# Kernel optimization log

Measured on AMD Instinct MI355X. Metric: run time of the kernel, lower is better.

The kernel has to match this reference:

```python
import jax, jax.numpy as jnp
import numpy as np

B, L, D, DF, E, R = 4, 1024, 1024, 4096, 32768, 64
EPS = 1e-6


def layer_norm(x, g, b, eps=EPS):
    mu = x.mean(-1, keepdims=True)
    var = ((x - mu) ** 2).mean(-1, keepdims=True)
    return (x - mu) * jax.lax.rsqrt(var + eps) * g + b


def setup_inputs() -> dict:
    key = jax.random.key(0)
    ks = jax.random.split(key, 16)
    s = 0.02
    return {
        "hidden_states": jax.random.normal(ks[0], (B, L, D), jnp.float32),
        "rel_table": jax.random.normal(ks[1], (R, D), jnp.float32) * s,
        "Wq": jax.random.normal(ks[2], (D, D), jnp.float32) * s,
        "bq": jnp.zeros((D,), jnp.float32),
        "Wk": jax.random.normal(ks[3], (D, D), jnp.float32) * s,
        "Wv": jax.random.normal(ks[4], (D, D), jnp.float32) * s,
        "Wo": jax.random.normal(ks[5], (D, D), jnp.float32) * s,
        "bo": jnp.zeros((D,), jnp.float32),
        "ln0_g": jnp.ones((D,), jnp.float32),
        "ln0_b": jnp.zeros((D,), jnp.float32),
        "ln1_g": jnp.ones((D,), jnp.float32),
        "ln1_b": jnp.zeros((D,), jnp.float32),
        "W1": jax.random.normal(ks[6], (D, DF), jnp.float32) * s,
        "b1": jnp.zeros((DF,), jnp.float32),
        "W2": jax.random.normal(ks[7], (DF, D), jnp.float32) * s,
        "b2": jnp.zeros((D,), jnp.float32),
        "ln2_g": jnp.ones((D,), jnp.float32),
        "ln2_b": jnp.zeros((D,), jnp.float32),
        "edge_src": jax.random.randint(ks[8], (B, E), 0, L, jnp.int32),
        "edge_dst": jax.random.randint(ks[9], (B, E), 0, L, jnp.int32),
        "edge_rel": jax.random.randint(ks[10], (B, E), 0, R, jnp.int32),
    }


def reference(hidden_states, rel_table, Wq, bq, Wk, Wv, Wo, bo,
              ln0_g, ln0_b, ln1_g, ln1_b, W1, b1, W2, b2, ln2_g, ln2_b,
              edge_src, edge_dst, edge_rel):
    scale = np.sqrt(D).astype(np.float32)  # num_heads=1 -> d_k = D
    hs_norm = layer_norm(hidden_states, ln0_g, ln0_b)

    def rgat_one(x, src, dst, rel):
        # x: [L, D]; src/dst/rel: [E]
        e = rel_table[rel]                       # [E, D] relation embeddings
        q = x @ Wq + bq
        k = x @ Wk
        v = x @ Wv
        score = jnp.sum((k[src] + e) * q[dst], axis=-1) / scale      # [E]
        score = jnp.exp(jnp.clip(score, -10.0, 10.0))
        wv = jax.ops.segment_sum((v[src] + e) * score[:, None], dst, num_segments=L)
        z = jax.ops.segment_sum(score, dst, num_segments=L)          # [L]
        o = wv / z[:, None]
        out = layer_norm(x + o @ Wo + bo, ln1_g, ln1_b)
        ffn = jnp.maximum(out @ W1 + b1, 0.0) @ W2 + b2
        return layer_norm(out + ffn, ln2_g, ln2_b)

    graph_rep = jax.vmap(rgat_one)(hs_norm, edge_src, edge_dst, edge_rel)
    out = jax.nn.elu(graph_rep)                  # dropout = identity (eval)
    return hidden_states + out
```

## Files before the change

kernel.cpp:

```cpp
#include <hip/hip_runtime.h>
#include <hip/hip_bf16.h>

#define B_SZ 4
#define L_SEQ 1024
#define D_MODEL 1024
#define DF_FF 4096
#define E_PER_B 32768
#define R_REL 64
#define M_ROWS (B_SZ * L_SEQ)

typedef __attribute__((ext_vector_type(8))) short bf16x8;
typedef __attribute__((ext_vector_type(4))) float f32x4;

__device__ inline float b2f(unsigned short u) {
    union { unsigned int i; float f; } x; x.i = ((unsigned int)u) << 16; return x.f;
}
__device__ inline unsigned short f2b(float f) {
    union { float f; unsigned int u; } x; x.f = f;
    unsigned int r = x.u + 0x7FFFu + ((x.u >> 16) & 1u);
    return (unsigned short)(r >> 16);
}

#define GLOBAL_CAST(p) ((const __attribute__((address_space(1))) void*)(p))
#define LDS_CAST(p)    ((__attribute__((address_space(3))) void*)(p))

#define BT_QKV (1024u * 3072u)
#define SEXT_M 1152
#define LDA_WV 1088
#define LDB_WVP 1152
#define BT_WVP (1024u * 1152u)

__global__ void prep_all(const float* __restrict__ Wq, const float* __restrict__ Wk,
                         const float* __restrict__ Wv, const float* __restrict__ Wo,
                         const float* __restrict__ W1, const float* __restrict__ W2,
                         const float* __restrict__ rel, const float* __restrict__ bq,
                         const float* __restrict__ hidden,
                         const float* __restrict__ ln0_g, const float* __restrict__ ln0_b,
                         unsigned short* __restrict__ Wqkv_t, unsigned short* __restrict__ Wo_t,
                         unsigned short* __restrict__ W1_t, unsigned short* __restrict__ W2_t,
                         unsigned short* __restrict__ relbPad,
                         float* __restrict__ bqkv,
                         unsigned short* __restrict__ Xn_b16,
                         float* __restrict__ zeroReg) {
    __shared__ float tile[32][33];
    __shared__ float sb1[4], sb2[4];
    const int id = blockIdx.x, tid = threadIdx.x;
    if (id < 12288) {
        const float* src; unsigned short* dst; int K, N, x, y;
        if (id < 4096) {
            const int seg = id >> 10, t = id & 1023;
            K = 1024; N = 1024; x = t & 31; y = t >> 5;
            src = (seg == 0) ? Wq : (seg == 1) ? Wk : (seg == 2) ? Wv : Wo;
            dst = (seg == 3) ? Wo_t : (Wqkv_t + (size_t)seg * 1048576);
        } else if (id < 8192) {
            const int t = id - 4096; K = 1024; N = 4096; x = t & 127; y = t >> 7;
            src = W1; dst = W1_t;
        } else {
            const int t = id - 8192; K = 4096; N = 1024; x = t & 31; y = t >> 5;
            src = W2; dst = W2_t;
        }
        const int n0 = x * 32, k0 = y * 32, tx = tid & 31, ty = tid >> 5;
#pragma unroll
        for (int r = 0; r < 32; r += 8)
            tile[ty + r][tx] = src[(size_t)(k0 + ty + r) * N + (n0 + tx)];
        __syncthreads();
#pragma unroll
        for (int r = 0; r < 32; r += 8)
            dst[(size_t)(n0 + ty + r) * K + (k0 + tx)] = f2b(tile[tx][ty + r]);
    } else if (id < 12800) {
        const int i = (id - 12288) * 256 + tid;
        relbPad[i] = (i < 65536) ? f2b(rel[i]) : (unsigned short)0;
    } else if (id < 12812) {
        const int i = (id - 12800) * 256 + tid;
        bqkv[i] = (i < 1024) ? bq[i] : 0.0f;
    } else if (id < 16908) {
        const int row = id - 12812, t = tid;
        const size_t base = (size_t)row * 1024 + t * 4;
        float4 xv = *(const float4*)(hidden + base);
        float x0 = xv.x, x1 = xv.y, x2 = xv.z, x3 = xv.w;
        float s = x0 + x1 + x2 + x3;
#pragma unroll
        for (int o = 32; o > 0; o >>= 1) s += __shfl_down(s, o);
        if ((t & 63) == 0) sb1[t >> 6] = s;
        __syncthreads();
        const float mu = (sb1[0] + sb1[1] + sb1[2] + sb1[3]) * (1.0f / 1024.0f);
        const float d0 = x0 - mu, d1 = x1 - mu, d2 = x2 - mu, d3 = x3 - mu;
        float s2 = d0 * d0 + d1 * d1 + d2 * d2 + d3 * d3;
#pragma unroll
        for (int o = 32; o > 0; o >>= 1) s2 += __shfl_down(s2, o);
        if ((t & 63) == 0) sb2[t >> 6] = s2;
        __syncthreads();
        const float var = (sb2[0] + sb2[1] + sb2[2] + sb2[3]) * (1.0f / 1024.0f);
        const float rstd = rsqrtf(var + 1e-6f);
        const float4 gv = *(const float4*)(ln0_g + t * 4);
        const float4 bv = *(const float4*)(ln0_b + t * 4);
        ushort4 ob;
        ob.x = f2b(d0 * rstd * gv.x + bv.x);
        ob.y = f2b(d1 * rstd * gv.y + bv.y);
        ob.z = f2b(d2 * rstd * gv.z + bv.z);
        ob.w = f2b(d3 * rstd * gv.w + bv.w);
        *(ushort4*)(Xn_b16 + base) = ob;
    } else {
        const size_t base = (size_t)(id - 16908) * 4096 + tid * 4;
        const float4 z4 = make_float4(0.f, 0.f, 0.f, 0.f);
#pragma unroll
        for (int j = 0; j < 4; j++)
            *(float4*)(zeroReg + base + j * 1024) = z4;
    }
}

__device__ inline void tile_swizzle(int id, int ntn, int& tm, int& tn) {
    tm = ((id & 7) + ((id >> 3) / ntn) * 8) * 128;
    tn = ((id >> 3) % ntn) * 128;
}
__device__ inline void tsw256(int id, int ntn, int& tm, int& tn) {
    tm = ((id & 7) + ((id >> 3) / ntn) * 8) * 256;
    tn = ((id >> 3) % ntn) * 256;
}

#define GEMM_BODY(GA, LDA_, GB, LDB_, KLEN)                                                 \
    f32x4 acc[4][4];                                                                        \
    _Pragma("unroll") for (int i = 0; i < 4; i++)                                           \
        _Pragma("unroll") for (int j = 0; j < 4; j++) acc[i][j] = (f32x4)0.0f;              \
    for (int k0 = 0; k0 < (KLEN); k0 += 64) {                                               \
        __syncthreads();                                                                    \
        _Pragma("unroll") for (int r = 0; r < 4; ++r) {                                     \
            __builtin_amdgcn_global_load_lds(GLOBAL_CAST((GA) + (size_t)r * 8 * (LDA_)),    \
                LDS_CAST(&lA[(wave * 32 + r * 8) * 64]), 16, 0, 0);                         \
            __builtin_amdgcn_global_load_lds(GLOBAL_CAST((GB) + (size_t)r * 8 * (LDB_)),    \
                LDS_CAST(&lB[(wave * 32 + r * 8) * 64]), 16, 0, 0);                         \
        }                                                                                   \
        (GA) += 64; (GB) += 64;                                                             \
        __builtin_amdgcn_s_waitcnt(0);                                                      \
        __syncthreads();                                                                    \
        _Pragma("unroll") for (int kk = 0; kk < 2; ++kk) {                                  \
            const int cb = kk * 4 + quad;                                                   \
            bf16x8 af[4], bf[4];                                                            \
            _Pragma("unroll") for (int i = 0; i < 4; i++) {                                 \
                const int ra = wm + i * 16 + l16;                                           \
                af[i] = *(const bf16x8*)&lA[ra * 64 + ((cb ^ (ra & 7)) * 8)];               \
                const int rb = wn + i * 16 + l16;                                           \
                bf[i] = *(const bf16x8*)&lB[rb * 64 + ((cb ^ (rb & 7)) * 8)];               \
            }                                                                               \
            _Pragma("unroll") for (int mi = 0; mi < 4; mi++)                                \
                _Pragma("unroll") for (int ni = 0; ni < 4; ni++)                            \
                    acc[mi][ni] = __builtin_amdgcn_mfma_f32_16x16x32_bf16(                  \
                        af[mi], bf[ni], acc[mi][ni], 0, 0, 0);                              \
        }                                                                                   \
    }

#define ST_Aq(bufc, QM, kt) { \
    _Pragma("unroll") for (int j_ = 0; j_ < 2; j_++) { \
        const int u_ = j_ * 8 + wv; \
        const int lr_ = ((u_ >> 3) * 128) + (QM) * 64 + ((u_ & 7) * 8); \
        __builtin_amdgcn_global_load_lds(GLOBAL_CAST(Ag + (size_t)lr_ * lda + (kt) * 64), \
            LDS_CAST(&ls[bufc][0][lr_ * 64]), 16, 0, 0); } }
#define ST_Bq(bufc, QN, kt) { \
    _Pragma("unroll") for (int j_ = 0; j_ < 2; j_++) { \
        const int u_ = j_ * 8 + wv; \
        const int lr_ = ((u_ >> 2) * 64) + (QN) * 32 + ((u_ & 3) * 8); \
        __builtin_amdgcn_global_load_lds(GLOBAL_CAST(Bg + (size_t)lr_ * ldb + (kt) * 64), \
            LDS_CAST(&ls[bufc][1][lr_ * 64]), 16, 0, 0); } }

#define RD_Af(bufc, QM) { \
    _Pragma("unroll") for (int m4_ = 0; m4_ < 4; m4_++) \
        _Pragma("unroll") for (int kk_ = 0; kk_ < 2; kk_++) \
            af[m4_][kk_] = *(const bf16x8*)&ls[bufc][0][ \
                (wm * 128 + (QM) * 64 + m4_ * 16 + l16) * 64 + (((kk_ * 4 + quad) ^ (l16 & 7)) * 8)]; }
#define RD_Bs(SLOT, bufc, QN) { \
    _Pragma("unroll") for (int n2_ = 0; n2_ < 2; n2_++) \
        _Pragma("unroll") for (int kk_ = 0; kk_ < 2; kk_++) \
            SLOT[n2_][kk_] = *(const bf16x8*)&ls[bufc][1][ \
                (wc * 64 + (QN) * 32 + n2_ * 16 + l16) * 64 + (((kk_ * 4 + quad) ^ (l16 & 7)) * 8)]; }

#define VM4 asm volatile("s_waitcnt vmcnt(4)" ::: "memory");
#define VM0 asm volatile("s_waitcnt vmcnt(0)" ::: "memory");

#define MMCL(QM, QN, BS) \
    __builtin_amdgcn_s_setprio(1); \
    _Pragma("unroll") for (int m4_ = 0; m4_ < 4; m4_++) \
        _Pragma("unroll") for (int n2_ = 0; n2_ < 2; n2_++) \
            _Pragma("unroll") for (int kk_ = 0; kk_ < 2; kk_++) \
                acc[(QM) * 4 + m4_][(QN) * 2 + n2_] = __builtin_amdgcn_mfma_f32_16x16x32_bf16( \
                    af[m4_][kk_], BS[n2_][kk_], acc[(QM) * 4 + m4_][(QN) * 2 + n2_], 0, 0, 0); \
    __builtin_amdgcn_s_setprio(0);

#define PH_R(bufc, QM, QN, BS, STMT, POST) { \
    STMT; \
    RD_Af(bufc, QM) \
    asm volatile("s_waitcnt lgkmcnt(0)" ::: "memory"); \
    __builtin_amdgcn_sched_barrier(0); \
    MMCL(QM, QN, BS) \
    POST; \
    __builtin_amdgcn_s_barrier(); }
#define PH_H(bufc, QM, QN, BS, STMT, POST) { \
    STMT; \
    __builtin_amdgcn_sched_barrier(0); \
    MMCL(QM, QN, BS) \
    POST; \
    __builtin_amdgcn_s_barrier(); }

template<bool RELU, bool SPLITK>
__global__ __launch_bounds__(512, 2)
void gemm256(const unsigned short* __restrict__ A, int lda,
             const unsigned short* __restrict__ Bt, int ldb,
             const float* __restrict__ bias,
             unsigned short* __restrict__ C, size_t pstride,
             int N, int Kc, int ntn) {
    __shared__ unsigned short ls[2][2][16384];
    int tile_m, tile_n;
    tsw256(blockIdx.x, ntn, tile_m, tile_n);
    const int t = threadIdx.x;
    const int wv = t >> 6, lane = t & 63;
    const int wm = wv >> 2;
    const int wc = wv & 3;
    const int quad = lane >> 4, l16 = lane & 15;
    const int srow8 = lane >> 3;
    const int schunk = ((lane & 7) ^ srow8) * 8;
    const int z = SPLITK ? blockIdx.z : 0;
    const int kofs = z * Kc;

    const unsigned short* Ag = A + (size_t)(tile_m + srow8) * lda + kofs + schunk;
    const unsigned short* Bg = Bt + (size_t)(tile_n + srow8) * ldb + kofs + schunk;

    f32x4 acc[8][4];
#pragma unroll
    for (int i = 0; i < 8; i++)
#pragma unroll
        for (int j = 0; j < 4; j++) acc[i][j] = (f32x4)0.0f;
    bf16x8 af[4][2], b0f[2][2], b1f[2][2];

    ST_Aq(0, 0, 0) ST_Aq(0, 1, 0) ST_Bq(0, 0, 0) ST_Bq(0, 1, 0)
    ST_Aq(1, 0, 1) ST_Bq(1, 1, 1) ST_Aq(1, 1, 1)
    asm volatile("s_waitcnt vmcnt(6)" ::: "memory");
    __builtin_amdgcn_s_barrier();
    RD_Bs(b0f, 0, 0) RD_Bs(b1f, 0, 1)

    const int NI = Kc >> 7;
    for (int it = 0; it < NI - 1; ++it) {
        const int t1 = 2 * it + 1, s0 = 2 * it + 2, s1 = 2 * it + 3;
        PH_R(0, 0, 0, b0f, ST_Bq(1, 0, t1), )
        PH_H(0, 0, 1, b1f, ST_Aq(0, 0, s0), )
        PH_R(0, 1, 1, b1f, ST_Bq(0, 1, s0), VM4 RD_Bs(b1f, 1, 1))
        PH_H(0, 1, 0, b0f, ST_Aq(0, 1, s0), RD_Bs(b0f, 1, 0))
        PH_R(1, 0, 0, b0f, ST_Bq(0, 0, s0), )
        PH_H(1, 0, 1, b1f, ST_Aq(1, 0, s1), )
        PH_R(1, 1, 1, b1f, ST_Bq(1, 1, s1), VM4 RD_Bs(b1f, 0, 1))
        PH_H(1, 1, 0, b0f, ST_Aq(1, 1, s1), RD_Bs(b0f, 0, 0))
    }
    {
        const int t1 = 2 * NI - 1;
        PH_R(0, 0, 0, b0f, ST_Bq(1, 0, t1), )
        PH_H(0, 0, 1, b1f, , )
        PH_R(0, 1, 1, b1f, , VM0 RD_Bs(b1f, 1, 1))
        PH_H(0, 1, 0, b0f, , RD_Bs(b0f, 1, 0))
        PH_R(1, 0, 0, b0f, , )
        PH_H(1, 0, 1, b1f, , )
        PH_R(1, 1, 1, b1f, , )
        PH_H(1, 1, 0, b0f, , )
    }

    unsigned short* Co = C + (SPLITK ? (size_t)z * pstride : 0);
#pragma unroll
    for (int mi = 0; mi < 8; mi++) {
#pragma unroll
        for (int ni = 0; ni < 4; ni++) {
            const int col = tile_n + wc * 64 + ni * 16 + l16;
            const float bv = (SPLITK && z != 0) ? 0.0f : bias[col];
#pragma unroll
            for (int r = 0; r < 4; r++) {
                const int row = tile_m + wm * 128 + mi * 16 + quad * 4 + r;
                float v = acc[mi][ni][r] + bv;
                if (RELU) v = fmaxf(v, 0.0f);
                Co[(size_t)row * N + col] = f2b(v);
            }
        }
    }
}

__global__ __launch_bounds__(256, 4)
void sext_w(const unsigned short* __restrict__ QKV,
            const unsigned short* __restrict__ relPad,
            const unsigned short* __restrict__ Wo_t,
            unsigned short* __restrict__ Pbase,
            unsigned short* __restrict__ Bwvp) {
    __shared__ unsigned short lA[128 * 64];
    __shared__ unsigned short lB[128 * 64];
    const int id = blockIdx.x, t = threadIdx.x;
    const int wave = t >> 6, lane = t & 63;
    const int wm = (wave >> 1) * 64, wn = (wave & 1) * 64;
    const int quad = lane >> 4, l16 = lane & 15;
    const int srow = lane >> 3;
    const int schunk = ((lane & 7) ^ srow) * 8;

    if (id >= 288) {
        const int t2 = id - 288;
        const int b = t2 / 72, rem = t2 % 72;
        const int tile_m = (rem / 9) * 128;
        const int tile_n = (rem % 9) * 128;
        const unsigned short* gA = Wo_t + (size_t)(tile_m + wave * 32 + srow) * 1024 + schunk;
        const int brow = tile_n + wave * 32 + srow;
        const unsigned short* gB;
        size_t ldb;
        if (tile_n < 1024) {
            gB = QKV + (size_t)b * BT_QKV + (size_t)brow * 3072 + 2048 + schunk;
            ldb = 3072;
        } else {
            gB = relPad + (size_t)(brow - 1024) * 1024 + schunk;
            ldb = 1024;
        }
        GEMM_BODY(gA, 1024, gB, ldb, 1024)
        unsigned short* P = Bwvp + (size_t)b * BT_WVP;
#pragma unroll
        for (int mi = 0; mi < 4; mi++) {
#pragma unroll
            for (int ni = 0; ni < 4; ni++) {
                const int col = tile_n + wn + ni * 16 + l16;
#pragma unroll
                for (int r = 0; r < 4; r++) {
                    const int row = tile_m + wm + mi * 16 + quad * 4 + r;
                    P[(size_t)row * LDB_WVP + col] = f2b(acc[mi][ni][r]);
                }
            }
        }
        return;
    }

    const int bx = id % 72, b = id / 72;
    const int tile_m = (bx >> 3) * 128;
    const int tile_n = (bx & 7) * 128;
    const int arow = tile_m + wave * 32 + srow;
    const unsigned short* gA;
    size_t lda;
    if (tile_m < 1024) {
        gA = QKV + (size_t)b * BT_QKV + (size_t)arow * 3072 + 1024 + schunk;
        lda = 3072;
    } else {
        gA = relPad + (size_t)(arow - 1024) * 1024 + schunk;
        lda = 1024;
    }
    const unsigned short* gB = QKV + (size_t)b * BT_QKV
                                   + (size_t)(tile_n + wave * 32 + srow) * 3072 + schunk;
    GEMM_BODY(gA, lda, gB, 3072, 1024)
    unsigned short* P = Pbase + (size_t)b * (SEXT_M * 1024);
#pragma unroll
    for (int mi = 0; mi < 4; mi++) {
#pragma unroll
        for (int ni = 0; ni < 4; ni++) {
            const int col = tile_n + wn + ni * 16 + l16;
#pragma unroll
            for (int r = 0; r < 4; r++) {
                const int row = tile_m + wm + mi * 16 + quad * 4 + r;
                P[(size_t)row * 1024 + col] = f2b(acc[mi][ni][r]);
            }
        }
    }
}

__global__ __launch_bounds__(256, 4)
void gemm_wv_splitk(const unsigned short* __restrict__ A,
                    const unsigned short* __restrict__ Bt,
                    const float* __restrict__ bias,
                    unsigned short* __restrict__ Pbase, size_t pstride) {
    __shared__ unsigned short lA[128 * 64];
    __shared__ unsigned short lB[128 * 64];
    int tile_m, tile_n;
    tile_swizzle(blockIdx.x, 8, tile_m, tile_n);
    const int z = blockIdx.z;
    const int kofs = z * 576;
    const int Kc = z ? 512 : 576;
    const int t = threadIdx.x;
    const int wave = t >> 6, lane = t & 63;
    const int wm = (wave >> 1) * 64, wn = (wave & 1) * 64;
    const int quad = lane >> 4, l16 = lane & 15;
    const int srow = lane >> 3;
    const int schunk = ((lane & 7) ^ srow) * 8;
    const unsigned short* gA = A + (size_t)(tile_m + wave * 32 + srow) * LDA_WV + kofs + schunk;
    const unsigned short* gB = Bt + (size_t)(tile_m >> 10) * BT_WVP
                                  + (size_t)(tile_n + wave * 32 + srow) * LDB_WVP + kofs + schunk;
    GEMM_BODY(gA, LDA_WV, gB, LDB_WVP, Kc)
    unsigned short* P = Pbase + (size_t)z * pstride;
#pragma unroll
    for (int mi = 0; mi < 4; mi++) {
#pragma unroll
        for (int ni = 0; ni < 4; ni++) {
            const int col = tile_n + wn + ni * 16 + l16;
            const float bv = (z == 0) ? bias[col] : 0.0f;
#pragma unroll
            for (int r = 0; r < 4; r++) {
                const int row = tile_m + wm + mi * 16 + quad * 4 + r;
                P[(size_t)row * 1024 + col] = f2b(acc[mi][ni][r] + bv);
            }
        }
    }
}

template<bool FINAL, int NR>
__global__ void ln_kernel(const unsigned short* __restrict__ Xb,
                          const unsigned short* __restrict__ Rbase, size_t rstride,
                          const float* __restrict__ g, const float* __restrict__ be,
                          unsigned short* __restrict__ ob16,
                          const float* __restrict__ hidden, float* __restrict__ fout) {
    __shared__ float sb1[4], sb2[4];
    const int row = blockIdx.x, t = threadIdx.x;
    const size_t base = (size_t)row * 1024 + t * 4;

    ushort4 xv = *(const ushort4*)(Xb + base);
    float x0 = b2f(xv.x), x1 = b2f(xv.y), x2 = b2f(xv.z), x3 = b2f(xv.w);
#pragma unroll
    for (int r = 0; r < NR; r++) {
        ushort4 rv = *(const ushort4*)(Rbase + r * rstride + base);
        x0 += b2f(rv.x); x1 += b2f(rv.y); x2 += b2f(rv.z); x3 += b2f(rv.w);
    }
    float s = x0 + x1 + x2 + x3;
#pragma unroll
    for (int o = 32; o > 0; o >>= 1) s += __shfl_down(s, o);
    if ((t & 63) == 0) sb1[t >> 6] = s;
    __syncthreads();
    const float mu = (sb1[0] + sb1[1] + sb1[2] + sb1[3]) * (1.0f / 1024.0f);

    const float d0 = x0 - mu, d1 = x1 - mu, d2 = x2 - mu, d3 = x3 - mu;
    float s2 = d0 * d0 + d1 * d1 + d2 * d2 + d3 * d3;
#pragma unroll
    for (int o = 32; o > 0; o >>= 1) s2 += __shfl_down(s2, o);
    if ((t & 63) == 0) sb2[t >> 6] = s2;
    __syncthreads();
    const float var = (sb2[0] + sb2[1] + sb2[2] + sb2[3]) * (1.0f / 1024.0f);
    const float rstd = rsqrtf(var + 1e-6f);

    const float4 gv = *(const float4*)(g + t * 4);
    const float4 bv = *(const float4*)(be + t * 4);
    const float y0 = d0 * rstd * gv.x + bv.x;
    const float y1 = d1 * rstd * gv.y + bv.y;
    const float y2 = d2 * rstd * gv.z + bv.z;
    const float y3 = d3 * rstd * gv.w + bv.w;

    if (!FINAL) {
        ushort4 ob; ob.x = f2b(y0); ob.y = f2b(y1); ob.z = f2b(y2); ob.w = f2b(y3);
        *(ushort4*)(ob16 + base) = ob;
    } else {
        const float4 hv = *(const float4*)(hidden + base);
        const float e0 = y0 > 0.0f ? y0 : expm1f(y0);
        const float e1 = y1 > 0.0f ? y1 : expm1f(y1);
        const float e2 = y2 > 0.0f ? y2 : expm1f(y2);
        const float e3 = y3 > 0.0f ? y3 : expm1f(y3);
        float4 o; o.x = hv.x + e0; o.y = hv.y + e1; o.z = hv.z + e2; o.w = hv.w + e3;
        *(float4*)(fout + base) = o;
    }
}

__global__ void edge_scatter(const unsigned short* __restrict__ S,
                             const int* __restrict__ src, const int* __restrict__ dst,
                             const int* __restrict__ rel,
                             float* __restrict__ A, float* __restrict__ G) {
    const int gg = blockIdx.x * 256 + threadIdx.x;
    const int b = gg >> 15;
    const int s = src[gg], d = dst[gg], r = rel[gg];
    const size_t sbase = ((size_t)b * SEXT_M + s) * 1024 + d;
    const size_t tbase = ((size_t)b * SEXT_M + 1024 + r) * 1024 + d;
    const float sval = b2f(S[sbase]);
    const float tval = b2f(S[tbase]);
    float sc = (sval + tval) * (1.0f / 32.0f);
    sc = expf(fminf(fmaxf(sc, -10.0f), 10.0f));
    atomicAdd(&A[((size_t)((b << 10) + d) << 10) + s], sc);
    atomicAdd(&G[((size_t)((b << 10) + d) << 6) + r], sc);
}

__global__ void normalize(const float* __restrict__ A, const float* __restrict__ G,
                          unsigned short* __restrict__ Awv) {
    __shared__ float sInv;
    const int row = blockIdx.x, t = threadIdx.x;
    float v = 0.0f;
    if (t < 64) {
        v = G[(size_t)row * 64 + t];
        float s = v;
#pragma unroll
        for (int o = 1; o < 64; o <<= 1) s += __shfl_xor(s, o);
        if (t == 0) sInv = 1.0f / s;
    }
    __syncthreads();
    const float inv = sInv;
    const size_t obase = (size_t)row * LDA_WV;
    const float4 a = *(const float4*)(A + (size_t)row * 1024 + t * 4);
    ushort4 o;
    o.x = f2b(a.x * inv); o.y = f2b(a.y * inv); o.z = f2b(a.z * inv); o.w = f2b(a.w * inv);
    *(ushort4*)(Awv + obase + t * 4) = o;
    if (t < 16) {
        const float4 gq = *(const float4*)(G + (size_t)row * 64 + t * 4);
        ushort4 og;
        og.x = f2b(gq.x * inv); og.y = f2b(gq.y * inv);
        og.z = f2b(gq.z * inv); og.w = f2b(gq.w * inv);
        *(ushort4*)(Awv + obase + 1024 + t * 4) = og;
    }
}

extern "C" void kernel_launch(void* const* d_in, const int* in_sizes, int n_in,
                              void* d_out, int out_size, void* d_ws, size_t ws_size,
                              hipStream_t stream) {
    const float* hidden  = (const float*)d_in[0];
    const float* rel_tbl = (const float*)d_in[1];
    const float* Wq = (const float*)d_in[2];
    const float* bq = (const float*)d_in[3];
    const float* Wk = (const float*)d_in[4];
    const float* Wv = (const float*)d_in[5];
    const float* Wo = (const float*)d_in[6];
    const float* bo = (const float*)d_in[7];
    const float* ln0_g = (const float*)d_in[8];
    const float* ln0_b = (const float*)d_in[9];
    const float* ln1_g = (const float*)d_in[10];
    const float* ln1_b = (const float*)d_in[11];
    const float* W1 = (const float*)d_in[12];
    const float* b1 = (const float*)d_in[13];
    const float* W2 = (const float*)d_in[14];
    const float* b2 = (const float*)d_in[15];
    const float* ln2_g = (const float*)d_in[16];
    const float* ln2_b = (const float*)d_in[17];
    const int* esrc = (const int*)d_in[18];
    const int* edst = (const int*)d_in[19];
    const int* erel = (const int*)d_in[20];
    float* out = (float*)d_out;

    char* ws = (char*)d_ws;
    const size_t MB = 1024 * 1024;
    unsigned short* Xn_b16  = (unsigned short*)(ws + 16 * MB);
    unsigned short* H1      = (unsigned short*)(ws + 0);
    unsigned short* Wqkv_t  = (unsigned short*)(ws + 24 * MB);
    unsigned short* Wo_t    = (unsigned short*)(ws + 30 * MB);
    unsigned short* W1_t    = (unsigned short*)(ws + 32 * MB);
    unsigned short* W2_t    = (unsigned short*)(ws + 40 * MB);
    unsigned short* relbPad = (unsigned short*)(ws + 48 * MB);
    float*          bqkv    = (float*)(ws + 48 * MB + 512 * 1024);
    unsigned short* QKV     = (unsigned short*)(ws + 49 * MB);
    unsigned short* Awv     = (unsigned short*)(ws + 49 * MB);
    unsigned short* Qw2H    = (unsigned short*)(ws + 49 * MB);
    unsigned short* PwoH    = (unsigned short*)(ws + 66 * MB);
    unsigned short* SxH     = (unsigned short*)(ws + 73 * MB);
    unsigned short* Bwvp    = (unsigned short*)(ws + 92 * MB);
    float*          Amat    = (float*)(ws + 101 * MB);
    float*          Gmat    = (float*)(ws + 117 * MB);
    unsigned short* Out_b16 = (unsigned short*)(ws + 113 * MB);

    const size_t PSTRIDE_H = 4u * 1024 * 1024;
    const dim3 blk(256);
    const dim3 blk512(512);

    prep_all<<<17996, blk, 0, stream>>>(Wq, Wk, Wv, Wo, W1, W2, rel_tbl, bq,
                                        hidden, ln0_g, ln0_b,
                                        Wqkv_t, Wo_t, W1_t, W2_t, relbPad, bqkv,
                                        Xn_b16, Amat);
    gemm256<false, false><<<dim3(192), blk512, 0, stream>>>(
        Xn_b16, 1024, Wqkv_t, 1024, bqkv, QKV, 0, 3072, 1024, 12);
    sext_w<<<576, blk, 0, stream>>>(QKV, relbPad, Wo_t, SxH, Bwvp);
    edge_scatter<<<512, blk, 0, stream>>>(SxH, esrc, edst, erel, Amat, Gmat);
    normalize<<<M_ROWS, blk, 0, stream>>>(Amat, Gmat, Awv);
    gemm_wv_splitk<<<dim3(256, 1, 2), blk, 0, stream>>>(Awv, Bwvp, bo, PwoH, PSTRIDE_H);
    ln_kernel<false, 2><<<M_ROWS, blk, 0, stream>>>(Xn_b16, PwoH, PSTRIDE_H, ln1_g, ln1_b,
                                                    Out_b16, nullptr, nullptr);
    gemm256<true, false><<<dim3(256), blk512, 0, stream>>>(
        Out_b16, 1024, W1_t, 1024, b1, H1, 0, 4096, 1024, 16);
    gemm256<false, true><<<dim3(64, 1, 4), blk512, 0, stream>>>(
        H1, 4096, W2_t, 4096, b2, Qw2H, PSTRIDE_H, 1024, 1024, 4);
    ln_kernel<true, 4><<<M_ROWS, blk, 0, stream>>>(Out_b16, Qw2H, PSTRIDE_H, ln2_g, ln2_b,
                                                   nullptr, hidden, out);
    (void)in_sizes; (void)n_in; (void)out_size; (void)ws_size;
}
```

Before: 348.6 us.

## Replace edge scatter with dst-bucketed gather and LDS accumulation

Result: slower. 358.4 us (+2.8%).

```diff
diff --git a/kernel.cpp b/kernel.cpp
--- a/kernel.cpp
+++ b/kernel.cpp
@@ -41,7 +41,7 @@
                          unsigned short* __restrict__ relbPad,
                          float* __restrict__ bqkv,
                          unsigned short* __restrict__ Xn_b16,
-                         float* __restrict__ zeroReg) {
+                         unsigned int* __restrict__ cnt) {
     __shared__ float tile[32][33];
     __shared__ float sb1[4], sb2[4];
     const int id = blockIdx.x, tid = threadIdx.x;
@@ -101,11 +101,98 @@
         ob.w = f2b(d3 * rstd * gv.w + bv.w);
         *(ushort4*)(Xn_b16 + base) = ob;
     } else {
-        const size_t base = (size_t)(id - 16908) * 4096 + tid * 4;
-        const float4 z4 = make_float4(0.f, 0.f, 0.f, 0.f);
+        uint4 z4; z4.x = z4.y = z4.z = z4.w = 0u;
 #pragma unroll
         for (int j = 0; j < 4; j++)
-            *(float4*)(zeroReg + base + j * 1024) = z4;
+            *(uint4*)(cnt + tid * 16 + j * 4) = z4;
+    }
+}
+
+__global__ void bucket_count(const int* __restrict__ dst, unsigned int* __restrict__ cnt) {
+    const int gg = blockIdx.x * 256 + threadIdx.x;
+    const int b = gg >> 15;
+    atomicAdd(&cnt[(b << 10) | dst[gg]], 1u);
+}
+
+__global__ void bucket_scan(const unsigned int* __restrict__ cnt,
+                            unsigned int* __restrict__ offs,
+                            unsigned int* __restrict__ cur) {
+    __shared__ unsigned int ps[1024];
+    const int t = threadIdx.x;
+    const unsigned int c0 = cnt[t * 4], c1 = cnt[t * 4 + 1];
+    const unsigned int c2 = cnt[t * 4 + 2], c3 = cnt[t * 4 + 3];
+    const unsigned int local = c0 + c1 + c2 + c3;
+    ps[t] = local;
+    __syncthreads();
+    for (int off = 1; off < 1024; off <<= 1) {
+        const unsigned int v = (t >= off) ? ps[t - off] : 0u;
+        __syncthreads();
+        ps[t] += v;
+        __syncthreads();
+    }
+    const unsigned int excl = ps[t] - local;
+    const unsigned int o0 = excl, o1 = o0 + c0, o2 = o1 + c1, o3 = o2 + c2;
+    offs[t * 4] = o0; offs[t * 4 + 1] = o1; offs[t * 4 + 2] = o2; offs[t * 4 + 3] = o3;
+    cur[t * 4] = o0;  cur[t * 4 + 1] = o1;  cur[t * 4 + 2] = o2;  cur[t * 4 + 3] = o3;
+}
+
+__global__ void bucket_fill(const int* __restrict__ src, const int* __restrict__ dst,
+                            const int* __restrict__ rel,
+                            unsigned int* __restrict__ cur, unsigned int* __restrict__ elist) {
+    const int gg = blockIdx.x * 256 + threadIdx.x;
+    const int b = gg >> 15;
+    const unsigned int pos = atomicAdd(&cur[(b << 10) | dst[gg]], 1u);
+    elist[pos] = (unsigned int)src[gg] | ((unsigned int)rel[gg] << 10);
+}
+
+__global__ void edge_gather(const unsigned short* __restrict__ S,
+                            const unsigned int* __restrict__ cnt,
+                            const unsigned int* __restrict__ offs,
+                            const unsigned int* __restrict__ elist,
+                            unsigned short* __restrict__ Awv) {
+    __shared__ float aRow[1024];
+    __shared__ float gRow[64];
+    __shared__ float sInvL;
+    const int bd = blockIdx.x;
+    const int b = bd >> 10, d = bd & 1023;
+    const int t = threadIdx.x;
+#pragma unroll
+    for (int j = 0; j < 4; j++) aRow[t * 4 + j] = 0.0f;
+    if (t < 64) gRow[t] = 0.0f;
+    __syncthreads();
+
+    const unsigned int n = cnt[bd];
+    const unsigned int base = offs[bd];
+    const size_t sB = (size_t)b * SEXT_M * 1024 + d;
+    for (unsigned int i = t; i < n; i += 256) {
+        const unsigned int e = elist[base + i];
+        const int s = e & 1023, r = e >> 10;
+        const float sval = b2f(S[sB + (size_t)s * 1024]);
+        const float tval = b2f(S[sB + (size_t)(1024 + r) * 1024]);
+        float sc = (sval + tval) * (1.0f / 32.0f);
+        sc = expf(fminf(fmaxf(sc, -10.0f), 10.0f));
+        atomicAdd(&aRow[s], sc);
+        atomicAdd(&gRow[r], sc);
+    }
+    __syncthreads();
+    if (t < 64) {
+        float s = gRow[t];
+#pragma unroll
+        for (int o = 1; o < 64; o <<= 1) s += __shfl_xor(s, o);
+        if (t == 0) sInvL = 1.0f / s;
+    }
+    __syncthreads();
+    const float inv = sInvL;
+    const size_t obase = (size_t)bd * LDA_WV;
+    ushort4 o;
+    o.x = f2b(aRow[t * 4] * inv);     o.y = f2b(aRow[t * 4 + 1] * inv);
+    o.z = f2b(aRow[t * 4 + 2] * inv); o.w = f2b(aRow[t * 4 + 3] * inv);
+    *(ushort4*)(Awv + obase + t * 4) = o;
+    if (t < 16) {
+        ushort4 og;
+        og.x = f2b(gRow[t * 4] * inv);     og.y = f2b(gRow[t * 4 + 1] * inv);
+        og.z = f2b(gRow[t * 4 + 2] * inv); og.w = f2b(gRow[t * 4 + 3] * inv);
+        *(ushort4*)(Awv + obase + 1024 + t * 4) = og;
     }
 }
 
@@ -449,51 +536,6 @@
     }
 }
 
-__global__ void edge_scatter(const unsigned short* __restrict__ S,
-                             const int* __restrict__ src, const int* __restrict__ dst,
-                             const int* __restrict__ rel,
-                             float* __restrict__ A, float* __restrict__ G) {
-    const int gg = blockIdx.x * 256 + threadIdx.x;
-    const int b = gg >> 15;
-    const int s = src[gg], d = dst[gg], r = rel[gg];
-    const size_t sbase = ((size_t)b * SEXT_M + s) * 1024 + d;
-    const size_t tbase = ((size_t)b * SEXT_M + 1024 + r) * 1024 + d;
-    const float sval = b2f(S[sbase]);
-    const float tval = b2f(S[tbase]);
-    float sc = (sval + tval) * (1.0f / 32.0f);
-    sc = expf(fminf(fmaxf(sc, -10.0f), 10.0f));
-    atomicAdd(&A[((size_t)((b << 10) + d) << 10) + s], sc);
-    atomicAdd(&G[((size_t)((b << 10) + d) << 6) + r], sc);
-}
-
-__global__ void normalize(const float* __restrict__ A, const float* __restrict__ G,
-                          unsigned short* __restrict__ Awv) {
-    __shared__ float sInv;
-    const int row = blockIdx.x, t = threadIdx.x;
-    float v = 0.0f;
-    if (t < 64) {
-        v = G[(size_t)row * 64 + t];
-        float s = v;
-#pragma unroll
-        for (int o = 1; o < 64; o <<= 1) s += __shfl_xor(s, o);
-        if (t == 0) sInv = 1.0f / s;
-    }
-    __syncthreads();
-    const float inv = sInv;
-    const size_t obase = (size_t)row * LDA_WV;
-    const float4 a = *(const float4*)(A + (size_t)row * 1024 + t * 4);
-    ushort4 o;
-    o.x = f2b(a.x * inv); o.y = f2b(a.y * inv); o.z = f2b(a.z * inv); o.w = f2b(a.w * inv);
-    *(ushort4*)(Awv + obase + t * 4) = o;
-    if (t < 16) {
-        const float4 gq = *(const float4*)(G + (size_t)row * 64 + t * 4);
-        ushort4 og;
-        og.x = f2b(gq.x * inv); og.y = f2b(gq.y * inv);
-        og.z = f2b(gq.z * inv); og.w = f2b(gq.w * inv);
-        *(ushort4*)(Awv + obase + 1024 + t * 4) = og;
-    }
-}
-
 extern "C" void kernel_launch(void* const* d_in, const int* in_sizes, int n_in,
                               void* d_out, int out_size, void* d_ws, size_t ws_size,
                               hipStream_t stream) {
@@ -536,23 +578,27 @@
     unsigned short* PwoH    = (unsigned short*)(ws + 66 * MB);
     unsigned short* SxH     = (unsigned short*)(ws + 73 * MB);
     unsigned short* Bwvp    = (unsigned short*)(ws + 92 * MB);
-    float*          Amat    = (float*)(ws + 101 * MB);
-    float*          Gmat    = (float*)(ws + 117 * MB);
+    unsigned int*   cnt     = (unsigned int*)(ws + 101 * MB);
+    unsigned int*   offs    = (unsigned int*)(ws + 101 * MB + 64 * 1024);
+    unsigned int*   cur     = (unsigned int*)(ws + 101 * MB + 128 * 1024);
+    unsigned int*   elist   = (unsigned int*)(ws + 101 * MB + 256 * 1024);
     unsigned short* Out_b16 = (unsigned short*)(ws + 113 * MB);
 
     const size_t PSTRIDE_H = 4u * 1024 * 1024;
     const dim3 blk(256);
     const dim3 blk512(512);
 
-    prep_all<<<17996, blk, 0, stream>>>(Wq, Wk, Wv, Wo, W1, W2, rel_tbl, bq,
+    prep_all<<<16909, blk, 0, stream>>>(Wq, Wk, Wv, Wo, W1, W2, rel_tbl, bq,
                                         hidden, ln0_g, ln0_b,
                                         Wqkv_t, Wo_t, W1_t, W2_t, relbPad, bqkv,
-                                        Xn_b16, Amat);
+                                        Xn_b16, cnt);
+    bucket_count<<<512, blk, 0, stream>>>(edst, cnt);
+    bucket_scan<<<1, dim3(1024), 0, stream>>>(cnt, offs, cur);
+    bucket_fill<<<512, blk, 0, stream>>>(esrc, edst, erel, cur, elist);
     gemm256<false, false><<<dim3(192), blk512, 0, stream>>>(
         Xn_b16, 1024, Wqkv_t, 1024, bqkv, QKV, 0, 3072, 1024, 12);
     sext_w<<<576, blk, 0, stream>>>(QKV, relbPad, Wo_t, SxH, Bwvp);
-    edge_scatter<<<512, blk, 0, stream>>>(SxH, esrc, edst, erel, Amat, Gmat);
-    normalize<<<M_ROWS, blk, 0, stream>>>(Amat, Gmat, Awv);
+    edge_gather<<<4096, blk, 0, stream>>>(SxH, cnt, offs, elist, Awv);
     gemm_wv_splitk<<<dim3(256, 1, 2), blk, 0, stream>>>(Awv, Bwvp, bo, PwoH, PSTRIDE_H);
     ln_kernel<false, 2><<<M_ROWS, blk, 0, stream>>>(Xn_b16, PwoH, PSTRIDE_H, ln1_g, ln1_b,
                                                     Out_b16, nullptr, nullptr);
```
